# Kernel tuning notes

Measured on AMD Instinct MI355X. Metric: run time of the kernel, lower is better.

Reference implementation:

```python
import jax, jax.numpy as jnp
import numpy as np

OUT_SIZE = 7
SAMPLE_NUM = 2
FINEST_SCALE = 56.0
STRIDES = (4, 8, 16, 32)
IMG_H, IMG_W = 800.0, 1216.0


def roi_align(feat, rois, out_size, spatial_scale, sr):
    """Vectorized RoIAlign (aligned=False / mmdet legacy semantics).
    feat: [B,C,H,W]; rois: [K,5] (batch_idx, x1, y1, x2, y2). Returns [K,C,out,out]."""
    B, C, H, W = feat.shape
    K = rois.shape[0]
    ft = jnp.transpose(feat, (0, 2, 3, 1))  # [B,H,W,C] for channel-last gathers
    b = rois[:, 0].astype(jnp.int32)
    x1 = rois[:, 1] * spatial_scale
    y1 = rois[:, 2] * spatial_scale
    x2 = rois[:, 3] * spatial_scale
    y2 = rois[:, 4] * spatial_scale
    roi_w = jnp.maximum(x2 - x1, 1.0)
    roi_h = jnp.maximum(y2 - y1, 1.0)
    bin_w = roi_w / out_size
    bin_h = roi_h / out_size
    G = out_size * sr  # sample grid points per spatial dim
    g = (jnp.arange(G, dtype=feat.dtype) + 0.5) / sr  # sub-bin centers in bin units
    ys = y1[:, None] + g[None, :] * bin_h[:, None]  # [K,G]
    xs = x1[:, None] + g[None, :] * bin_w[:, None]  # [K,G]
    # validity (points outside [-1, H]/[-1, W] contribute 0)
    vy = (ys >= -1.0) & (ys <= H)
    vx = (xs >= -1.0) & (xs <= W)
    valid = vy[:, :, None] & vx[:, None, :]  # [K,G,G]
    # clamp into the map, then bilinear interpolate
    ysc = jnp.clip(ys, 0.0, H - 1)
    xsc = jnp.clip(xs, 0.0, W - 1)
    y0 = jnp.floor(ysc)
    x0 = jnp.floor(xsc)
    ly = ysc - y0
    lx = xsc - x0
    y0i = y0.astype(jnp.int32)
    x0i = x0.astype(jnp.int32)

    def gather(yi, xi):  # yi:[K,G], xi:[K,G] -> [K,G,G,C]
        yc = jnp.clip(yi, 0, H - 1)
        xc = jnp.clip(xi, 0, W - 1)
        return ft[b[:, None, None], yc[:, :, None], xc[:, None, :], :]

    wy0 = (1.0 - ly)[:, :, None, None]
    wy1 = ly[:, :, None, None]
    wx0 = (1.0 - lx)[:, None, :, None]
    wx1 = lx[:, None, :, None]
    val = (gather(y0i, x0i) * (wy0 * wx0)
           + gather(y0i, x0i + 1) * (wy0 * wx1)
           + gather(y0i + 1, x0i) * (wy1 * wx0)
           + gather(y0i + 1, x0i + 1) * (wy1 * wx1))  # [K,G,G,C]
    val = val * valid[..., None]
    # average the sr x sr samples in each output bin
    val = val.reshape(K, out_size, sr, out_size, sr, C).mean(axis=(2, 4))
    return jnp.transpose(val, (0, 3, 1, 2))  # [K,C,out,out]


def map_roi_levels(rois, num_levels):
    scale = jnp.sqrt((rois[:, 3] - rois[:, 1] + 1.0) * (rois[:, 4] - rois[:, 2] + 1.0))
    lvl = jnp.floor(jnp.log2(scale / FINEST_SCALE + 1e-6))
    return jnp.clip(lvl, 0, num_levels - 1).astype(jnp.int32)


def setup_inputs() -> dict:
    key = jax.random.key(0)
    ks = jax.random.split(key, 10)
    feat0 = jax.random.normal(ks[0], (2, 256, 200, 304), dtype=jnp.float32)
    feat1 = jax.random.normal(ks[1], (2, 256, 100, 152), dtype=jnp.float32)
    feat2 = jax.random.normal(ks[2], (2, 256, 50, 76), dtype=jnp.float32)
    feat3 = jax.random.normal(ks[3], (2, 256, 25, 38), dtype=jnp.float32)
    K = 1024
    b = jax.random.randint(ks[4], (K,), 0, 2).astype(jnp.float32)
    # log-uniform box sizes in [16, 600] px so all 4 FPN levels are used
    logw = jax.random.uniform(ks[5], (K,), minval=np.log(16.0), maxval=np.log(600.0))
    logh = jax.random.uniform(ks[6], (K,), minval=np.log(16.0), maxval=np.log(600.0))
    w = jnp.exp(logw)
    h = jnp.exp(logh)
    cx = jax.random.uniform(ks[7], (K,), minval=0.0, maxval=IMG_W)
    cy = jax.random.uniform(ks[8], (K,), minval=0.0, maxval=IMG_H)
    x1 = jnp.clip(cx - w / 2, 0.0, IMG_W - 2.0)
    y1 = jnp.clip(cy - h / 2, 0.0, IMG_H - 2.0)
    x2 = jnp.clip(cx + w / 2, x1 + 1.0, IMG_W - 1.0)
    y2 = jnp.clip(cy + h / 2, y1 + 1.0, IMG_H - 1.0)
    rois = jnp.stack([b, x1, y1, x2, y2], axis=1).astype(jnp.float32)
    return {"feat0": feat0, "feat1": feat1, "feat2": feat2, "feat3": feat3, "rois": rois}


def reference(feat0, feat1, feat2, feat3, rois):
    feats = [feat0, feat1, feat2, feat3]
    num_levels = len(feats)
    lvls = map_roi_levels(rois, num_levels)  # [K]
    K = rois.shape[0]
    C = feats[0].shape[1]
    out = jnp.zeros((K, C, OUT_SIZE, OUT_SIZE), dtype=feats[0].dtype)
    for i in range(num_levels):
        pooled = roi_align(feats[i], rois, OUT_SIZE, 1.0 / STRIDES[i], SAMPLE_NUM)
        out = out + jnp.where((lvls == i)[:, None, None, None], pooled, 0.0)
    return out
```

## Files before the change

### kernel.cpp

```cpp
#include <hip/hip_runtime.h>
#include <math.h>


#define OUT_SZ 7
#define NCH 256
#define NBINS 49
#define CGC 64
#define NGROUPS 4
#define LDS_N 1920

template<int VSH>
__device__ __forceinline__ void roi_group(
    const float* __restrict__ cbase, int CLrel, int HW, int H, int W,
    float x1, float y1, float bw, float bh,
    int t, float* __restrict__ outk, float (*lds)[LDS_N])
{
    const int V = 1 << VSH;
    const float fH = (float)H, fW = (float)W;

    float xf0 = fminf(fmaxf(x1 + 0.25f * bw, 0.0f), fW - 1.0f);
    float xfl = fminf(fmaxf(x1 + 6.75f * bw, 0.0f), fW - 1.0f);
    int xa = (int)floorf(xf0);
    int xb = min((int)floorf(xfl) + 1, W - 1);
    float yf0 = fminf(fmaxf(y1 + 0.25f * bh, 0.0f), fH - 1.0f);
    float yfl = fminf(fmaxf(y1 + 6.75f * bh, 0.0f), fH - 1.0f);
    int ya = (int)floorf(yf0);
    int yb = min((int)floorf(yfl) + 1, H - 1);

    int axa    = xa & ~(V - 1);
    int cpr    = ((xb - axa) >> VSH) + 1;
    int rowlen = cpr << VSH;
    int stride = rowlen + (((rowlen & 31) == 0) ? V : 0);
    int Rows   = yb - ya + 1;
    int C      = Rows * cpr;

    {
        int sent = Rows * stride;
        if (t == 0) { lds[0][sent] = 0.0f; lds[1][sent] = 0.0f; }
        int padw = stride - rowlen;
        if (padw) {
            int np = Rows * padw;
            for (int z = t; z < np; z += 256) {
                int zr = z / padw, zc = z - zr * padw;
                int idx = zr * stride + rowlen + zc;
                lds[0][idx] = 0.0f;
                lds[1][idx] = 0.0f;
            }
        }
    }

    int q0 = (t + 60) & 255;
    int goff[2], loff[2];
    bool act[2];
#pragma unroll
    for (int i = 0; i < 2; ++i) {
        int q = q0 + 256 * i;
        act[i] = q < C;
        int qq = act[i] ? q : 0;
        int r  = qq / cpr;
        int j  = qq - r * cpr;
        int rowbase = (ya + r) * W;
        int rel  = rowbase + axa + (j << VSH);
        int relc = min(rel, CLrel);
        goff[i] = relc;
        loff[i] = r * stride + (relc - rowbase - axa);
    }

    int bin = t >> 2;
    int s   = t & 3;
    int oy  = bin / OUT_SZ;
    int ox  = bin - oy * OUT_SZ;

    float xs  = x1 + ((float)(2 * ox + (s & 1)) + 0.5f) * 0.5f * bw;
    float ysv = y1 + ((float)(2 * oy + (s >> 1)) + 0.5f) * 0.5f * bh;
    bool vall = (xs >= -1.0f) && (xs <= fW) && (ysv >= -1.0f) && (ysv <= fH);

    float xc = fminf(fmaxf(xs, 0.0f), fW - 1.0f);
    float yc = fminf(fmaxf(ysv, 0.0f), fH - 1.0f);
    float xflr = floorf(xc), yflr = floorf(yc);
    int x0 = (int)xflr, y0 = (int)yflr;
    float lx = xc - xflr, ly = yc - yflr;

    int p0 = (y0 - ya) * stride + (x0 - axa);
    int ry = min(y0 + 1 - ya, Rows - 1);
    int p1 = ry * stride + (x0 - axa);

    float w00 = (1.0f - ly) * (1.0f - lx);
    float w01 = (1.0f - ly) * lx;
    float w10 = ly * (1.0f - lx);
    float w11 = ly * lx;

    auto ldchunk = [&](const float* p, int i) -> float4 {
        if (!act[i]) return make_float4(0.f, 0.f, 0.f, 0.f);
        if (VSH == 2) return *(const float4*)(p + goff[i]);
        float2 h2 = *(const float2*)(p + goff[i]);
        return make_float4(h2.x, h2.y, 0.f, 0.f);
    };
    auto stchunk = [&](float* dst, int i, float4 v) {
        if (act[i]) {
            if (VSH == 2) *(float4*)(dst + loff[i]) = v;
            else          *(float2*)(dst + loff[i]) = make_float2(v.x, v.y);
        }
    };

    float4 pvA[2], pvB[2], t0[2];
    t0[0]  = ldchunk(cbase, 0);
    pvA[0] = ldchunk(cbase + (size_t)HW, 0);
    pvB[0] = ldchunk(cbase + 2 * (size_t)HW, 0);
    if (C > 256) {
        t0[1]  = ldchunk(cbase, 1);
        pvA[1] = ldchunk(cbase + (size_t)HW, 1);
        pvB[1] = ldchunk(cbase + 2 * (size_t)HW, 1);
    }
    stchunk(lds[0], 0, t0[0]);
    if (C > 256) stchunk(lds[0], 1, t0[1]);
    __syncthreads();

    for (int c = 0; c < CGC; ++c) {
        if (c + 1 < CGC) {
            float* dst = lds[(c + 1) & 1];
            float4* src = ((c + 1) & 1) ? pvA : pvB;
            stchunk(dst, 0, src[0]);
            if (C > 256) stchunk(dst, 1, src[1]);
        }
        if (c + 3 < CGC) {
            const float* pn = cbase + (size_t)(c + 3) * HW;
            float4* dr = ((c + 3) & 1) ? pvA : pvB;
            dr[0] = ldchunk(pn, 0);
            if (C > 256) dr[1] = ldchunk(pn, 1);
        }
        if (t < 196) {
            const float* L = lds[c & 1];
            float v00 = L[p0];
            float v01 = L[p0 + 1];
            float v10 = L[p1];
            float v11 = L[p1 + 1];
            float val = vall ? (v00 * w00 + v01 * w01 + v10 * w10 + v11 * w11)
                             : 0.0f;
            val += __shfl_xor(val, 1, 64);
            val += __shfl_xor(val, 2, 64);
            if (s == 0) outk[c * NBINS + bin] = val * 0.25f;
        }
        __syncthreads();
    }
}

__global__ __launch_bounds__(256)
void roi_align_fused(const float* __restrict__ f0, const float* __restrict__ f1,
                     const float* __restrict__ f2, const float* __restrict__ f3,
                     const float* __restrict__ rois,
                     float* __restrict__ out)
{
    __shared__ __align__(16) float lds[2][LDS_N];

    const int k = blockIdx.x;
    const int g = blockIdx.y;
    const int t = threadIdx.x;

    float rb   = rois[k * 5 + 0];
    float rix1 = rois[k * 5 + 1];
    float riy1 = rois[k * 5 + 2];
    float rix2 = rois[k * 5 + 3];
    float riy2 = rois[k * 5 + 4];

    float scale = sqrtf((rix2 - rix1 + 1.0f) * (riy2 - riy1 + 1.0f));
    int lvl = (int)floorf(log2f(scale * (1.0f / 56.0f) + 1e-6f));
    lvl = lvl < 0 ? 0 : (lvl > 3 ? 3 : lvl);

    float ss = 1.0f / (float)(4 << lvl);
    float x1 = rix1 * ss, y1 = riy1 * ss;
    float rw = fmaxf(rix2 * ss - x1, 1.0f);
    float rh = fmaxf(riy2 * ss - y1, 1.0f);
    float bw = rw * (1.0f / OUT_SZ);
    float bh = rh * (1.0f / OUT_SZ);
    const int H = 800  >> (2 + lvl);
    const int W = 1216 >> (2 + lvl);

    const float* fb = (lvl == 0) ? f0 : (lvl == 1) ? f1 : (lvl == 2) ? f2 : f3;
    const int HW  = H * W;
    const int TOT = 2 * NCH * HW;
    const int base_off = ((int)rb * NCH + g * CGC) * HW;
    const float* cbase = fb + base_off;
    float* outk = out + ((size_t)k * NCH + (size_t)(g * CGC)) * NBINS;

    if (W & 3) {
        int CLrel = TOT - base_off - (CGC - 1) * HW - 2;
        roi_group<1>(cbase, CLrel, HW, H, W, x1, y1, bw, bh, t, outk, lds);
    } else {
        int CLrel = TOT - base_off - (CGC - 1) * HW - 4;
        roi_group<2>(cbase, CLrel, HW, H, W, x1, y1, bw, bh, t, outk, lds);
    }
}

extern "C" void kernel_launch(void* const* d_in, const int* in_sizes, int n_in,
                              void* d_out, int out_size, void* d_ws, size_t ws_size,
                              hipStream_t stream)
{
    const float* f0   = (const float*)d_in[0];
    const float* f1   = (const float*)d_in[1];
    const float* f2   = (const float*)d_in[2];
    const float* f3   = (const float*)d_in[3];
    const float* rois = (const float*)d_in[4];
    float* out = (float*)d_out;

    int K = in_sizes[4] / 5;
    if (K <= 0) return;

    roi_align_fused<<<dim3(K, NGROUPS), 256, 0, stream>>>(f0, f1, f2, f3, rois, out);
}
```

Baseline: 310.8 us.

## Replace LDS-staged RoI tile pipeline with direct per-lane global gathers

Drops the double-buffered LDS staging of the RoI bounding patch per channel and instead has each wave handle one channel at a time, with 49 lanes each gathering their 16 bilinear taps straight from global memory and computing all four samples of a bin in registers. This removes the barriers, the LDS traffic and the cross-lane shuffle reduction, and raises occupancy through launch bounds. In exchange, the global loads become scattered and uncoalesced, 15 of 64 lanes sit idle, and results now depend on caches to absorb the repeated taps. Clamping x0 to W-2 and y0 to H-2 changes the edge handling to an equivalent form.

```diff
diff --git a/kernel.cpp b/kernel.cpp
--- a/kernel.cpp
+++ b/kernel.cpp
@@ -5,157 +5,19 @@
 #define OUT_SZ 7
 #define NCH 256
 #define NBINS 49
-#define CGC 64
 #define NGROUPS 4
-#define LDS_N 1920
 
-template<int VSH>
-__device__ __forceinline__ void roi_group(
-    const float* __restrict__ cbase, int CLrel, int HW, int H, int W,
-    float x1, float y1, float bw, float bh,
-    int t, float* __restrict__ outk, float (*lds)[LDS_N])
+__global__ __launch_bounds__(256, 6)
+void roi_align_direct(const float* __restrict__ f0, const float* __restrict__ f1,
+                      const float* __restrict__ f2, const float* __restrict__ f3,
+                      const float* __restrict__ rois,
+                      float* __restrict__ out)
 {
-    const int V = 1 << VSH;
-    const float fH = (float)H, fW = (float)W;
-
-    float xf0 = fminf(fmaxf(x1 + 0.25f * bw, 0.0f), fW - 1.0f);
-    float xfl = fminf(fmaxf(x1 + 6.75f * bw, 0.0f), fW - 1.0f);
-    int xa = (int)floorf(xf0);
-    int xb = min((int)floorf(xfl) + 1, W - 1);
-    float yf0 = fminf(fmaxf(y1 + 0.25f * bh, 0.0f), fH - 1.0f);
-    float yfl = fminf(fmaxf(y1 + 6.75f * bh, 0.0f), fH - 1.0f);
-    int ya = (int)floorf(yf0);
-    int yb = min((int)floorf(yfl) + 1, H - 1);
-
-    int axa    = xa & ~(V - 1);
-    int cpr    = ((xb - axa) >> VSH) + 1;
-    int rowlen = cpr << VSH;
-    int stride = rowlen + (((rowlen & 31) == 0) ? V : 0);
-    int Rows   = yb - ya + 1;
-    int C      = Rows * cpr;
-
-    {
-        int sent = Rows * stride;
-        if (t == 0) { lds[0][sent] = 0.0f; lds[1][sent] = 0.0f; }
-        int padw = stride - rowlen;
-        if (padw) {
-            int np = Rows * padw;
-            for (int z = t; z < np; z += 256) {
-                int zr = z / padw, zc = z - zr * padw;
-                int idx = zr * stride + rowlen + zc;
-                lds[0][idx] = 0.0f;
-                lds[1][idx] = 0.0f;
-            }
-        }
-    }
-
-    int q0 = (t + 60) & 255;
-    int goff[2], loff[2];
-    bool act[2];
-#pragma unroll
-    for (int i = 0; i < 2; ++i) {
-        int q = q0 + 256 * i;
-        act[i] = q < C;
-        int qq = act[i] ? q : 0;
-        int r  = qq / cpr;
-        int j  = qq - r * cpr;
-        int rowbase = (ya + r) * W;
-        int rel  = rowbase + axa + (j << VSH);
-        int relc = min(rel, CLrel);
-        goff[i] = relc;
-        loff[i] = r * stride + (relc - rowbase - axa);
-    }
-
-    int bin = t >> 2;
-    int s   = t & 3;
-    int oy  = bin / OUT_SZ;
-    int ox  = bin - oy * OUT_SZ;
-
-    float xs  = x1 + ((float)(2 * ox + (s & 1)) + 0.5f) * 0.5f * bw;
-    float ysv = y1 + ((float)(2 * oy + (s >> 1)) + 0.5f) * 0.5f * bh;
-    bool vall = (xs >= -1.0f) && (xs <= fW) && (ysv >= -1.0f) && (ysv <= fH);
-
-    float xc = fminf(fmaxf(xs, 0.0f), fW - 1.0f);
-    float yc = fminf(fmaxf(ysv, 0.0f), fH - 1.0f);
-    float xflr = floorf(xc), yflr = floorf(yc);
-    int x0 = (int)xflr, y0 = (int)yflr;
-    float lx = xc - xflr, ly = yc - yflr;
-
-    int p0 = (y0 - ya) * stride + (x0 - axa);
-    int ry = min(y0 + 1 - ya, Rows - 1);
-    int p1 = ry * stride + (x0 - axa);
-
-    float w00 = (1.0f - ly) * (1.0f - lx);
-    float w01 = (1.0f - ly) * lx;
-    float w10 = ly * (1.0f - lx);
-    float w11 = ly * lx;
-
-    auto ldchunk = [&](const float* p, int i) -> float4 {
-        if (!act[i]) return make_float4(0.f, 0.f, 0.f, 0.f);
-        if (VSH == 2) return *(const float4*)(p + goff[i]);
-        float2 h2 = *(const float2*)(p + goff[i]);
-        return make_float4(h2.x, h2.y, 0.f, 0.f);
-    };
-    auto stchunk = [&](float* dst, int i, float4 v) {
-        if (act[i]) {
-            if (VSH == 2) *(float4*)(dst + loff[i]) = v;
-            else          *(float2*)(dst + loff[i]) = make_float2(v.x, v.y);
-        }
-    };
-
-    float4 pvA[2], pvB[2], t0[2];
-    t0[0]  = ldchunk(cbase, 0);
-    pvA[0] = ldchunk(cbase + (size_t)HW, 0);
-    pvB[0] = ldchunk(cbase + 2 * (size_t)HW, 0);
-    if (C > 256) {
-        t0[1]  = ldchunk(cbase, 1);
-        pvA[1] = ldchunk(cbase + (size_t)HW, 1);
-        pvB[1] = ldchunk(cbase + 2 * (size_t)HW, 1);
-    }
-    stchunk(lds[0], 0, t0[0]);
-    if (C > 256) stchunk(lds[0], 1, t0[1]);
-    __syncthreads();
-
-    for (int c = 0; c < CGC; ++c) {
-        if (c + 1 < CGC) {
-            float* dst = lds[(c + 1) & 1];
-            float4* src = ((c + 1) & 1) ? pvA : pvB;
-            stchunk(dst, 0, src[0]);
-            if (C > 256) stchunk(dst, 1, src[1]);
-        }
-        if (c + 3 < CGC) {
-            const float* pn = cbase + (size_t)(c + 3) * HW;
-            float4* dr = ((c + 3) & 1) ? pvA : pvB;
-            dr[0] = ldchunk(pn, 0);
-            if (C > 256) dr[1] = ldchunk(pn, 1);
-        }
-        if (t < 196) {
-            const float* L = lds[c & 1];
-            float v00 = L[p0];
-            float v01 = L[p0 + 1];
-            float v10 = L[p1];
-            float v11 = L[p1 + 1];
-            float val = vall ? (v00 * w00 + v01 * w01 + v10 * w10 + v11 * w11)
-                             : 0.0f;
-            val += __shfl_xor(val, 1, 64);
-            val += __shfl_xor(val, 2, 64);
-            if (s == 0) outk[c * NBINS + bin] = val * 0.25f;
-        }
-        __syncthreads();
-    }
-}
-
-__global__ __launch_bounds__(256)
-void roi_align_fused(const float* __restrict__ f0, const float* __restrict__ f1,
-                     const float* __restrict__ f2, const float* __restrict__ f3,
-                     const float* __restrict__ rois,
-                     float* __restrict__ out)
-{
-    __shared__ __align__(16) float lds[2][LDS_N];
-
     const int k = blockIdx.x;
     const int g = blockIdx.y;
     const int t = threadIdx.x;
+    const int w    = t >> 6;
+    const int lane = t & 63;
 
     float rb   = rois[k * 5 + 0];
     float rix1 = rois[k * 5 + 1];
@@ -175,20 +37,75 @@
     float bh = rh * (1.0f / OUT_SZ);
     const int H = 800  >> (2 + lvl);
     const int W = 1216 >> (2 + lvl);
+    const float fH = (float)H, fW = (float)W;
+    const float* fb = (lvl == 0) ? f0 : (lvl == 1) ? f1 : (lvl == 2) ? f2 : f3;
+    const int HW = H * W;
 
-    const float* fb = (lvl == 0) ? f0 : (lvl == 1) ? f1 : (lvl == 2) ? f2 : f3;
-    const int HW  = H * W;
-    const int TOT = 2 * NCH * HW;
-    const int base_off = ((int)rb * NCH + g * CGC) * HW;
-    const float* cbase = fb + base_off;
-    float* outk = out + ((size_t)k * NCH + (size_t)(g * CGC)) * NBINS;
+    if (lane >= NBINS) return;
+    const int bin = lane;
+    const int oy = bin / OUT_SZ;
+    const int ox = bin - oy * OUT_SZ;
 
-    if (W & 3) {
-        int CLrel = TOT - base_off - (CGC - 1) * HW - 2;
-        roi_group<1>(cbase, CLrel, HW, H, W, x1, y1, bw, bh, t, outk, lds);
-    } else {
-        int CLrel = TOT - base_off - (CGC - 1) * HW - 4;
-        roi_group<2>(cbase, CLrel, HW, H, W, x1, y1, bw, bh, t, outk, lds);
+    float lx[2], fvx[2]; int cx[2];
+#pragma unroll
+    for (int j = 0; j < 2; ++j) {
+        float xs = x1 + ((float)(2 * ox + j) + 0.5f) * 0.5f * bw;
+        fvx[j] = (xs >= -1.0f && xs <= fW) ? 1.0f : 0.0f;
+        float xc = fminf(fmaxf(xs, 0.0f), fW - 1.0f);
+        int x0 = (int)floorf(xc);
+        x0 = min(x0, W - 2);
+        lx[j] = xc - (float)x0;
+        cx[j] = x0;
+    }
+    float ly[2], fvy[2]; int ry[2];
+#pragma unroll
+    for (int i = 0; i < 2; ++i) {
+        float ysv = y1 + ((float)(2 * oy + i) + 0.5f) * 0.5f * bh;
+        fvy[i] = (ysv >= -1.0f && ysv <= fH) ? 1.0f : 0.0f;
+        float yc = fminf(fmaxf(ysv, 0.0f), fH - 1.0f);
+        int y0 = (int)floorf(yc);
+        y0 = min(y0, H - 2);
+        ly[i] = yc - (float)y0;
+        ry[i] = y0;
+    }
+    float wv00 = fvy[0] * fvx[0], wv01 = fvy[0] * fvx[1];
+    float wv10 = fvy[1] * fvx[0], wv11 = fvy[1] * fvx[1];
+
+    int off[8];
+#pragma unroll
+    for (int r = 0; r < 4; ++r) {
+        int row = ry[r >> 1] + (r & 1);
+        off[2 * r + 0] = row * W + cx[0];
+        off[2 * r + 1] = row * W + cx[1];
+    }
+
+    const int ch0 = g * 64 + w;
+    const float* chp = fb + (size_t)((int)rb * NCH + ch0) * HW;
+    float* outp = out + ((size_t)k * NCH + ch0) * NBINS + bin;
+
+#pragma unroll 2
+    for (int i = 0; i < 16; ++i) {
+        float v0[8], v1[8];
+#pragma unroll
+        for (int q = 0; q < 8; ++q) {
+            v0[q] = chp[off[q]];
+            v1[q] = chp[off[q] + 1];
+        }
+        float h[8];
+#pragma unroll
+        for (int q = 0; q < 8; ++q)
+            h[q] = fmaf(lx[q & 1], v1[q] - v0[q], v0[q]);
+
+        float s00 = fmaf(ly[0], h[2] - h[0], h[0]);
+        float s01 = fmaf(ly[0], h[3] - h[1], h[1]);
+        float s10 = fmaf(ly[1], h[6] - h[4], h[4]);
+        float s11 = fmaf(ly[1], h[7] - h[5], h[5]);
+
+        float acc = wv00 * s00 + wv01 * s01 + wv10 * s10 + wv11 * s11;
+        *outp = acc * 0.25f;
+
+        chp  += 4 * (size_t)HW;
+        outp += 4 * NBINS;
     }
 }
 
@@ -206,5 +123,5 @@
     int K = in_sizes[4] / 5;
     if (K <= 0) return;
 
-    roi_align_fused<<<dim3(K, NGROUPS), 256, 0, stream>>>(f0, f1, f2, f3, rois, out);
+    roi_align_direct<<<dim3(K, NGROUPS), 256, 0, stream>>>(f0, f1, f2, f3, rois, out);
 }
```

Result: no change. 304.8 us (-1.9%).
